# Kernel optimization log

Measured on AMD Instinct MI355X. Metric: run time of the kernel, lower is better.

## Reference

```python
import jax, jax.numpy as jnp
import numpy as np

B, T = 16, 40
NH, DEPTH, NCLASS, IMG_H, W_IMG = 128, 2, 6625, 32, 512
HIDDEN = 64  # nh < 256 -> hidden = 64
LINEAR_IN = NH * 8  # nh * int((32-3-1)/4+1)
BN_EPS = 1e-5


def _conv2d(x, w, b, stride, pad, groups=1):
    y = jax.lax.conv_general_dilated(
        x, w, (stride, stride), [(pad, pad), (pad, pad)],
        dimension_numbers=('NCHW', 'OIHW', 'NCHW'), feature_group_count=groups)
    return y + b[None, :, None, None]


def _conv_bn_act(x, w, b, g, bb, m, v, stride, pad, groups=1):
    y = _conv2d(x, w, b, stride, pad, groups)
    y = (y - m[None, :, None, None]) * jax.lax.rsqrt(v[None, :, None, None] + BN_EPS) \
        * g[None, :, None, None] + bb[None, :, None, None]
    return jax.nn.gelu(y, approximate=False)  # torch nn.GELU default = exact erf


def _gru(xs, wih, whh, bih, bhh):
    # torch GRU gate order: r, z, n. xs: [B, T, D] -> ys: [B, T, H]
    H = whh.shape[1]
    xp = jnp.einsum('btd,gd->btg', xs, wih) + bih  # [B,T,3H]

    def step(h, xt):
        hp = h @ whh.T + bhh
        r = jax.nn.sigmoid(xt[:, :H] + hp[:, :H])
        z = jax.nn.sigmoid(xt[:, H:2 * H] + hp[:, H:2 * H])
        n = jnp.tanh(xt[:, 2 * H:] + r * hp[:, 2 * H:])
        hn = (1.0 - z) * n + z * h
        return hn, hn

    h0 = jnp.zeros((xs.shape[0], H), xs.dtype)
    _, ys = jax.lax.scan(step, h0, jnp.swapaxes(xp, 0, 1))
    return jnp.swapaxes(ys, 0, 1)


def _forward(x, targets,
             conv0_w, conv0_b, bn0_g, bn0_b, bn0_m, bn0_v,
             blk_dw_w, blk_dw_b, blk_bn1_g, blk_bn1_b, blk_bn1_m, blk_bn1_v,
             blk_pw_w, blk_pw_b, blk_bn2_g, blk_bn2_b, blk_bn2_m, blk_bn2_v,
             enc_wih, enc_whh, enc_bih, enc_bhh,
             dec_wih, dec_whh, dec_bih, dec_bhh,
             emb, q_w, q_b, k_w, k_b, e_w, e_b, fc_w, fc_b):
    h = _conv_bn_act(x, conv0_w, conv0_b, bn0_g, bn0_b, bn0_m, bn0_v, 4, 0)  # [B,NH,8,128]
    # NOTE: original code applies each MicroBlock to the SAME x (feat = block(x)); faithful here.
    feat = h
    for i in range(DEPTH):
        t = h + _conv_bn_act(h, blk_dw_w[i], blk_dw_b[i], blk_bn1_g[i], blk_bn1_b[i],
                             blk_bn1_m[i], blk_bn1_v[i], 1, 1, groups=NH)
        feat = _conv_bn_act(t, blk_pw_w[i], blk_pw_b[i], blk_bn2_g[i], blk_bn2_b[i],
                            blk_bn2_m[i], blk_bn2_v[i], 1, 0)
    Bq, C, Hf, Wf = feat.shape
    feat_v = feat.reshape(Bq, C * Hf, Wf)  # Flatten(1,2)
    # adaptive_avg_pool1d target = W/4 == Wf -> identity
    feat_v = jnp.transpose(feat_v, (0, 2, 1))  # [B, Wf, C*Hf]
    enc = _gru(feat_v, enc_wih, enc_whh, enc_bih, enc_bhh)  # [B,Wf,H]
    out_enc = enc[:, -1:, :]  # [B,1,H]
    tgt = emb[targets]  # [B,T,H]
    in_dec = jnp.concatenate([out_enc, tgt], axis=1)  # [B,T+1,H]
    y = _gru(in_dec, dec_wih, dec_whh, dec_bih, dec_bhh)  # [B,T+1,H]
    q = y @ q_w.T + q_b  # [B,Td,NH]
    k = _conv2d(feat, k_w, k_b, 1, 1)  # [B,NH,h,w]
    t2 = jnp.tanh(k[:, None] + q[:, :, :, None, None])  # [B,Td,NH,h,w]
    e = jnp.einsum('btchw,c->bthw', t2, e_w[0]) + e_b[0]  # conv1x1_2: Linear(NH,1)
    a = jax.nn.softmax(e.reshape(Bq, e.shape[1], -1), axis=-1).reshape(e.shape)
    attn_feat = jnp.einsum('bchw,bthw->btc', feat, a)  # [B,Td,NH]
    # dropout: eval mode -> identity
    return attn_feat @ fc_w.T + fc_b  # [B,Td,NCLASS]


def setup_inputs() -> dict:
    key = jax.random.key(0)
    ks = iter(jax.random.split(key, 64))

    def rn(shape, s=0.05):
        return jax.random.normal(next(ks), shape, jnp.float32) * s

    inp = {
        'x': jax.random.normal(next(ks), (B, 3, IMG_H, W_IMG), jnp.float32),
        'targets': jax.random.randint(next(ks), (B, T), 0, NCLASS),
        'conv0_w': rn((NH, 3, 4, 4)), 'conv0_b': rn((NH,)),
        'bn0_g': jnp.ones((NH,)), 'bn0_b': jnp.zeros((NH,)),
        'bn0_m': jnp.zeros((NH,)), 'bn0_v': jnp.ones((NH,)),
        'blk_dw_w': rn((DEPTH, NH, 1, 3, 3)), 'blk_dw_b': rn((DEPTH, NH)),
        'blk_bn1_g': jnp.ones((DEPTH, NH)), 'blk_bn1_b': jnp.zeros((DEPTH, NH)),
        'blk_bn1_m': jnp.zeros((DEPTH, NH)), 'blk_bn1_v': jnp.ones((DEPTH, NH)),
        'blk_pw_w': rn((DEPTH, NH, NH, 1, 1)), 'blk_pw_b': rn((DEPTH, NH)),
        'blk_bn2_g': jnp.ones((DEPTH, NH)), 'blk_bn2_b': jnp.zeros((DEPTH, NH)),
        'blk_bn2_m': jnp.zeros((DEPTH, NH)), 'blk_bn2_v': jnp.ones((DEPTH, NH)),
        'enc_wih': rn((3 * HIDDEN, LINEAR_IN)), 'enc_whh': rn((3 * HIDDEN, HIDDEN)),
        'enc_bih': jnp.zeros((3 * HIDDEN,)), 'enc_bhh': jnp.zeros((3 * HIDDEN,)),
        'dec_wih': rn((3 * HIDDEN, HIDDEN)), 'dec_whh': rn((3 * HIDDEN, HIDDEN)),
        'dec_bih': jnp.zeros((3 * HIDDEN,)), 'dec_bhh': jnp.zeros((3 * HIDDEN,)),
        'emb': rn((NCLASS, HIDDEN)).at[1].set(0.0),  # padding_idx=1
        'q_w': rn((NH, HIDDEN)), 'q_b': jnp.zeros((NH,)),
        'k_w': rn((NH, NH, 3, 3)), 'k_b': jnp.zeros((NH,)),
        'e_w': rn((1, NH)), 'e_b': jnp.zeros((1,)),
        'fc_w': rn((NCLASS, NH)), 'fc_b': jnp.zeros((NCLASS,)),
    }
    return inp


def reference(x, targets,
              conv0_w, conv0_b, bn0_g, bn0_b, bn0_m, bn0_v,
              blk_dw_w, blk_dw_b, blk_bn1_g, blk_bn1_b, blk_bn1_m, blk_bn1_v,
              blk_pw_w, blk_pw_b, blk_bn2_g, blk_bn2_b, blk_bn2_m, blk_bn2_v,
              enc_wih, enc_whh, enc_bih, enc_bhh,
              dec_wih, dec_whh, dec_bih, dec_bhh,
              emb, q_w, q_b, k_w, k_b, e_w, e_b, fc_w, fc_b):
    return _forward(x, targets,
                    conv0_w, conv0_b, bn0_g, bn0_b, bn0_m, bn0_v,
                    blk_dw_w, blk_dw_b, blk_bn1_g, blk_bn1_b, blk_bn1_m, blk_bn1_v,
                    blk_pw_w, blk_pw_b, blk_bn2_g, blk_bn2_b, blk_bn2_m, blk_bn2_v,
                    enc_wih, enc_whh, enc_bih, enc_bhh,
                    dec_wih, dec_whh, dec_bih, dec_bhh,
                    emb, q_w, q_b, k_w, k_b, e_w, e_b, fc_w, fc_b)
```

## Files before the change

### kernel.cpp

```cpp
#include <hip/hip_runtime.h>
#include <hip/hip_bf16.h>

#define DEV __device__ __forceinline__

#define B_    16
#define T_    40
#define TDEC  41
#define NH    128
#define HF    8
#define WF    128
#define HID   64
#define G3    192
#define NCLS  6625
#define SPAT  1024
#define NFRAG 415

typedef _Float16 half8 __attribute__((ext_vector_type(8)));
typedef _Float16 half2_ __attribute__((ext_vector_type(2)));
typedef float    f32x4 __attribute__((ext_vector_type(4)));
typedef float    f32x2 __attribute__((ext_vector_type(2)));

#if __has_builtin(__builtin_amdgcn_fdot2)
#define FDOT2(w,h,acc) __builtin_amdgcn_fdot2((w),(h),(acc),false)
#else
#define FDOT2(w,h,acc) ((acc) + (float)((w)[0])*(float)((h)[0]) + (float)((w)[1])*(float)((h)[1]))
#endif

DEV float sigmoidf_(float x){ return 1.0f/(1.0f + __expf(-x)); }
DEV float tanhf_(float x){ float e = __expf(2.0f*x); return 1.0f - 2.0f/(e + 1.0f); }
DEV float gelu_(float x){ return 0.5f*x*(1.0f + erff(x*0.70710678118654752f)); }
DEV float bnf_(float x, float g, float b, float m, float v){
  return (x - m)*rsqrtf(v + 1e-5f)*g + b;
}

__global__ __launch_bounds__(256) void k_conv0(const float* __restrict__ x,
    const float* __restrict__ w, const float* __restrict__ bias,
    const float* __restrict__ bng, const float* __restrict__ bnb,
    const float* __restrict__ bnm, const float* __restrict__ bnv,
    float* __restrict__ h)
{
  int tid = blockIdx.x*256 + threadIdx.x;
  int ow = tid & 127;
  int oh = (tid >> 7) & 7;
  int c4 = (tid >> 10) & 31;
  int b  = tid >> 15;
  float acc[4] = {0.f,0.f,0.f,0.f};
  int xbase = ((b*3)*32 + oh*4)*512 + ow*4;
  for (int ci = 0; ci < 3; ++ci){
    #pragma unroll
    for (int kh = 0; kh < 4; ++kh){
      float4 xv = *(const float4*)(x + xbase + ci*(32*512) + kh*512);
      #pragma unroll
      for (int cc = 0; cc < 4; ++cc){
        int co = c4*4 + cc;
        const float* wp = w + ((co*3 + ci)*4 + kh)*4;
        acc[cc] += xv.x*wp[0] + xv.y*wp[1] + xv.z*wp[2] + xv.w*wp[3];
      }
    }
  }
  #pragma unroll
  for (int cc = 0; cc < 4; ++cc){
    int co = c4*4 + cc;
    float v = acc[cc] + bias[co];
    v = bnf_(v, bng[co], bnb[co], bnm[co], bnv[co]);
    h[((b*NH + co)*HF + oh)*WF + ow] = gelu_(v);
  }
}

__global__ __launch_bounds__(256) void k_dw(const float* __restrict__ h,
    const float* __restrict__ dww, const float* __restrict__ dwb,
    const float* __restrict__ g1, const float* __restrict__ b1,
    const float* __restrict__ m1, const float* __restrict__ v1,
    float* __restrict__ t)
{
  int tid = blockIdx.x*256 + threadIdx.x;
  int ow = tid & 127;
  int oh = (tid >> 7) & 7;
  int c  = (tid >> 10) & 127;
  int b  = tid >> 17;
  const float* wp = dww + NH*9 + c*9;
  const float* hp = h + ((b*NH + c)*HF)*WF;
  float acc = 0.f;
  #pragma unroll
  for (int kh = 0; kh < 3; ++kh){
    int ih = oh + kh - 1;
    if (ih < 0 || ih >= HF) continue;
    #pragma unroll
    for (int kw = 0; kw < 3; ++kw){
      int iw = ow + kw - 1;
      if (iw < 0 || iw >= WF) continue;
      acc += hp[ih*WF + iw]*wp[kh*3 + kw];
    }
  }
  float val = acc + dwb[NH + c];
  val = bnf_(val, g1[NH + c], b1[NH + c], m1[NH + c], v1[NH + c]);
  t[tid] = hp[oh*WF + ow] + gelu_(val);
}

__global__ __launch_bounds__(256) void k_fcprep(const float* __restrict__ fcw,
    _Float16* __restrict__ fcwH, _Float16* __restrict__ fcwL)
{
  int tid = blockIdx.x*256 + threadIdx.x;
  if (tid >= NFRAG*4*64*8) return;
  int j  = tid & 7;
  int l  = (tid >> 3) & 63;
  int kf = (tid >> 9) & 3;
  int nf = tid >> 11;
  int n = nf*16 + (l & 15);
  int k = kf*32 + ((l >> 4) << 3) + j;
  float v = (n < NCLS) ? fcw[n*NH + k] : 0.f;
  _Float16 hi = (_Float16)v;
  fcwH[tid] = hi;
  fcwL[tid] = (_Float16)(v - (float)hi);
}

__global__ __launch_bounds__(256) void k_misc(const float* __restrict__ pw,
    float* __restrict__ pwT, const float* __restrict__ kw,
    _Float16* __restrict__ kwA, const int* __restrict__ tgt,
    const float* __restrict__ emb, float* __restrict__ indec,
    const float* __restrict__ encwhh, unsigned* __restrict__ enc16,
    const float* __restrict__ decwhh, unsigned* __restrict__ dec16)
{
  int bid = blockIdx.x;
  if (bid < 64){
    int tid = bid*256 + threadIdx.x;
    int ci = tid & 127; int co = tid >> 7;
    pwT[ci*128 + co] = pw[16384 + co*128 + ci];
  } else if (bid < 640){
    int tid = (bid - 64)*256 + threadIdx.x;
    int j = tid & 7;
    int l = (tid >> 3) & 63;
    int f = (tid >> 9) & 7;
    int s = tid >> 12;
    int co = f*16 + (l & 15);
    int k  = s*32 + ((l >> 4) << 3) + j;
    int r  = k >> 7;
    int ci = k & 127;
    kwA[tid] = (_Float16)kw[(co*128 + ci)*9 + r];
  } else if (bid < 800){
    int tid = (bid - 640)*256 + threadIdx.x;
    if (tid >= B_*T_*HID) return;
    int j = tid & 63; int rest = tid >> 6;
    int t = rest % T_; int b = rest / T_;
    int cls = tgt[b*T_ + t];
    indec[(b*TDEC + 1 + t)*HID + j] = emb[cls*HID + j];
  } else {
    int seg = bid - 800;
    const float* src = (seg < 24) ? encwhh : decwhh;
    unsigned* dst    = (seg < 24) ? enc16   : dec16;
    int tid = (seg % 24)*256 + threadIdx.x;
    int r = tid >> 5; int k2 = tid & 31;
    half2_ hv;
    hv[0] = (_Float16)src[r*HID + 2*k2];
    hv[1] = (_Float16)src[r*HID + 2*k2 + 1];
    dst[tid] = __builtin_bit_cast(unsigned, hv);
  }
}

__global__ __launch_bounds__(512) void k_pw(const float* __restrict__ t,
    const float* __restrict__ pwT, const float* __restrict__ pwb,
    const float* __restrict__ g2, const float* __restrict__ b2,
    const float* __restrict__ m2, const float* __restrict__ v2,
    float* __restrict__ feat)
{
  int bid = blockIdx.x;
  int wh = bid & 1; int oh = (bid >> 1) & 7; int b = bid >> 4;
  int w0 = wh*64;
  int tid = threadIdx.x;
  __shared__ __align__(16) float tile[128*64];
  for (int i = 0; i < 16; ++i){
    int e = i*512 + tid; int ci = e >> 6; int wloc = e & 63;
    tile[ci*64 + wloc] = t[((b*NH + ci)*HF + oh)*WF + w0 + wloc];
  }
  __syncthreads();
  int co = tid & 127; int wq = tid >> 7;
  float acc[16];
  #pragma unroll
  for (int i = 0; i < 16; ++i) acc[i] = 0.f;
  for (int ci = 0; ci < 128; ++ci){
    float wt = pwT[ci*128 + co];
    const float4* tp = (const float4*)(tile + ci*64 + wq*16);
    #pragma unroll
    for (int j = 0; j < 4; ++j){
      float4 tv = tp[j];
      acc[j*4+0] += tv.x*wt; acc[j*4+1] += tv.y*wt;
      acc[j*4+2] += tv.z*wt; acc[j*4+3] += tv.w*wt;
    }
  }
  float bb = pwb[128 + co];
  float gg = g2[128 + co], bc = b2[128 + co], mm = m2[128 + co], vv = v2[128 + co];
  float* op = feat + ((b*NH + co)*HF + oh)*WF + w0 + wq*16;
  #pragma unroll
  for (int i = 0; i < 16; ++i){
    float v = bnf_(acc[i] + bb, gg, bc, mm, vv);
    op[i] = gelu_(v);
  }
}

__global__ __launch_bounds__(256) void k_encxp(const float* __restrict__ feat,
    const float* __restrict__ wih, const float* __restrict__ bih,
    float* __restrict__ xp)
{
  int m0 = blockIdx.x*32;
  int n0 = blockIdx.y*48;
  int b  = m0 >> 7;
  int w0 = m0 & 127;
  int tid = threadIdx.x;
  __shared__ float As[64*33];
  __shared__ float Bs[64*49];
  int tx = tid & 15, ty = tid >> 4;
  float acc[2][3] = {{0.f,0.f,0.f},{0.f,0.f,0.f}};
  for (int kt = 0; kt < 16; ++kt){
    int k0 = kt*64;
    #pragma unroll
    for (int i = 0; i < 8; ++i){
      int e = i*256 + tid; int kd = e >> 5; int mi = e & 31;
      int kg = k0 + kd;
      As[kd*33 + mi] = feat[((b*NH + (kg >> 3))*HF + (kg & 7))*WF + w0 + mi];
    }
    #pragma unroll
    for (int i = 0; i < 12; ++i){
      int e = i*256 + tid; int gi = e >> 6; int kd = e & 63;
      Bs[kd*49 + gi] = wih[(n0 + gi)*1024 + k0 + kd];
    }
    __syncthreads();
    for (int kd = 0; kd < 64; ++kd){
      float a0 = As[kd*33 + ty*2], a1 = As[kd*33 + ty*2 + 1];
      float b0 = Bs[kd*49 + tx*3], b1 = Bs[kd*49 + tx*3 + 1], b2 = Bs[kd*49 + tx*3 + 2];
      acc[0][0] += a0*b0; acc[0][1] += a0*b1; acc[0][2] += a0*b2;
      acc[1][0] += a1*b0; acc[1][1] += a1*b1; acc[1][2] += a1*b2;
    }
    __syncthreads();
  }
  #pragma unroll
  for (int i = 0; i < 2; ++i){
    int m = m0 + ty*2 + i;
    #pragma unroll
    for (int j = 0; j < 3; ++j){
      int g = n0 + tx*3 + j;
      xp[m*G3 + g] = acc[i][j] + bih[g];
    }
  }
}

template<int STEPS, bool WRITE_ALL>
__global__ __attribute__((amdgpu_waves_per_eu(1, 1))) __launch_bounds__(64)
void k_scan2(const float* __restrict__ xp, const uint4* __restrict__ whh16,
             const float* __restrict__ bhh, float* __restrict__ outp)
{
  __shared__ __align__(16) _Float16 hsh16[HID];
  int g = threadIdx.x;
  int b = blockIdx.x;
  uint4 w0q[8], w1q[8], w2q[8];
  const uint4* q0 = whh16 + g*8;
  const uint4* q1 = whh16 + (HID + g)*8;
  const uint4* q2 = whh16 + (2*HID + g)*8;
  #pragma unroll
  for (int k = 0; k < 8; ++k){ w0q[k] = q0[k]; w1q[k] = q1[k]; w2q[k] = q2[k]; }
  float b0 = bhh[g], b1 = bhh[HID + g], b2 = bhh[2*HID + g];
  float hg = 0.f;
  hsh16[g] = (_Float16)0.f;
  const float* xpb = xp + b*STEPS*G3;
  float x0a = xpb[g], x1a = xpb[HID + g], x2a = xpb[2*HID + g];
  float x0b = 0.f, x1b = 0.f, x2b = 0.f;
  if (STEPS > 1){
    const float* p = xpb + G3 + g;
    x0b = p[0]; x1b = p[HID]; x2b = p[2*HID];
  }
  for (int t = 0; t < STEPS; ++t){
    float x0c = 0.f, x1c = 0.f, x2c = 0.f;
    if (t + 2 < STEPS){
      const float* p = xpb + (t + 2)*G3 + g;
      x0c = p[0]; x1c = p[HID]; x2c = p[2*HID];
    }
    const uint4* h4 = (const uint4*)hsh16;
    float a0 = b0, a1 = b1, a2 = b2;
    float d0 = 0.f, d1 = 0.f, d2 = 0.f;
    #pragma unroll
    for (int i = 0; i < 8; i += 2){
      uint4 hvA = h4[i], hvB = h4[i+1];
      #define DO4(hv, wq, aa, bb, cc)                                          \
      { half2_ h0 = __builtin_bit_cast(half2_, hv.x);                          \
        half2_ h1 = __builtin_bit_cast(half2_, hv.y);                          \
        half2_ h2 = __builtin_bit_cast(half2_, hv.z);                          \
        half2_ h3 = __builtin_bit_cast(half2_, hv.w);                          \
        aa = FDOT2(__builtin_bit_cast(half2_, w0q[wq].x), h0, aa);             \
        bb = FDOT2(__builtin_bit_cast(half2_, w1q[wq].x), h0, bb);             \
        cc = FDOT2(__builtin_bit_cast(half2_, w2q[wq].x), h0, cc);             \
        aa = FDOT2(__builtin_bit_cast(half2_, w0q[wq].y), h1, aa);             \
        bb = FDOT2(__builtin_bit_cast(half2_, w1q[wq].y), h1, bb);             \
        cc = FDOT2(__builtin_bit_cast(half2_, w2q[wq].y), h1, cc);             \
        aa = FDOT2(__builtin_bit_cast(half2_, w0q[wq].z), h2, aa);             \
        bb = FDOT2(__builtin_bit_cast(half2_, w1q[wq].z), h2, bb);             \
        cc = FDOT2(__builtin_bit_cast(half2_, w2q[wq].z), h2, cc);             \
        aa = FDOT2(__builtin_bit_cast(half2_, w0q[wq].w), h3, aa);             \
        bb = FDOT2(__builtin_bit_cast(half2_, w1q[wq].w), h3, bb);             \
        cc = FDOT2(__builtin_bit_cast(half2_, w2q[wq].w), h3, cc); }
      DO4(hvA, i,   a0, a1, a2)
      DO4(hvB, i+1, d0, d1, d2)
      #undef DO4
    }
    float hp0 = a0 + d0;
    float hp1 = a1 + d1;
    float hp2 = a2 + d2;
    float e0 = __expf(-(x0a + hp0));
    float r  = __builtin_amdgcn_rcpf(1.0f + e0);
    float e1 = __expf(-(x1a + hp1));
    float z  = __builtin_amdgcn_rcpf(1.0f + e1);
    float ag = x2a + r*hp2;
    float ex = __expf(2.0f*ag);
    float n  = 1.0f - 2.0f*__builtin_amdgcn_rcpf(ex + 1.0f);
    hg = z*(hg - n) + n;
    if (WRITE_ALL) outp[(b*TDEC + t)*HID + g] = hg;
    hsh16[g] = (_Float16)hg;
    x0a = x0b; x1a = x1b; x2a = x2b;
    x0b = x0c; x1b = x1c; x2b = x2c;
  }
  if (!WRITE_ALL) outp[(b*TDEC)*HID + g] = hg;
}

__global__ __launch_bounds__(64) void k_kconv3(const float* __restrict__ feat,
    const uint4* __restrict__ kwA4, const float* __restrict__ kb,
    float* __restrict__ ko)
{
  int bid = blockIdx.x;
  int b  = ((bid & 7) << 1) | ((bid >> 3) & 1);
  int mq = (bid >> 4) & 3;
  int cs = (bid >> 6) & 3;
  int wq = (bid >> 8) & 1;
  int oh = (bid >> 9) & 7;
  int l  = threadIdx.x;
  int w0 = wq*64 + mq*16;
  int iwb = w0 + (l & 15);
  int cib = (l >> 4) << 3;

  f32x4 acc0{0.f,0.f,0.f,0.f}, acc1{0.f,0.f,0.f,0.f};
  uint4 a0A, a0B, a1A, a1B;
  float b0v[8], b1v[8];

  #define ISS(s, aX, aY, bvv) {                                               \
    aX = kwA4[(s)*512 + cs*128 + l];                                          \
    aY = kwA4[(s)*512 + cs*128 + 64 + l];                                     \
    int r = (s) >> 2; int dh = r/3 - 1; int dw2 = r%3 - 1;                    \
    int ci0 = ((s) & 3) << 5;                                                 \
    int ih = oh + dh; int iw = iwb + dw2;                                     \
    bool ok = (ih >= 0) & (ih < HF) & (iw >= 0) & (iw < WF);                  \
    const float* fp = feat + ((b*NH + ci0 + cib)*HF + ih)*WF + iw;            \
    _Pragma("unroll")                                                         \
    for (int jj = 0; jj < 8; ++jj) bvv[jj] = ok ? fp[jj*(HF*WF)] : 0.f;       \
  }
  #define CMP(aX, aY, bvv) {                                                  \
    half8 bf;                                                                 \
    _Pragma("unroll")                                                         \
    for (int jj = 0; jj < 8; ++jj) bf[jj] = (_Float16)bvv[jj];                \
    half8 af0 = __builtin_bit_cast(half8, aX);                                \
    half8 af1 = __builtin_bit_cast(half8, aY);                                \
    acc0 = __builtin_amdgcn_mfma_f32_16x16x32_f16(af0, bf, acc0, 0, 0, 0);    \
    acc1 = __builtin_amdgcn_mfma_f32_16x16x32_f16(af1, bf, acc1, 0, 0, 0);    \
  }

  ISS(0, a0A, a0B, b0v);
  for (int s = 0; s < 36; s += 2){
    if (s + 1 < 36) ISS(s + 1, a1A, a1B, b1v);
    CMP(a0A, a0B, b0v);
    if (s + 2 < 36) ISS(s + 2, a0A, a0B, b0v);
    if (s + 1 < 36) CMP(a1A, a1B, b1v);
  }
  #undef ISS
  #undef CMP

  int m = w0 + (l & 15);
  #pragma unroll
  for (int q = 0; q < 4; ++q){
    int co0 = cs*32 + ((l >> 4) << 2) + q;
    int co1 = co0 + 16;
    ko[((b*NH + co0)*HF + oh)*WF + m] = acc0[q] + kb[co0];
    ko[((b*NH + co1)*HF + oh)*WF + m] = acc1[q] + kb[co1];
  }
}

__global__ void k_xpd(const float* __restrict__ indec, const float* __restrict__ wih,
                      const float* __restrict__ bih, float* __restrict__ xpd)
{
  int tid = blockIdx.x*256 + threadIdx.x;
  if (tid >= B_*TDEC*G3) return;
  int g = tid % G3; int bt = tid / G3;
  const float4* r4 = (const float4*)(indec + bt*HID);
  const float4* w4 = (const float4*)(wih + g*HID);
  float acc = bih[g];
  #pragma unroll
  for (int j = 0; j < 16; ++j){
    float4 rv = r4[j], wv = w4[j];
    acc += rv.x*wv.x + rv.y*wv.y + rv.z*wv.z + rv.w*wv.w;
  }
  xpd[tid] = acc;
}

__global__ void k_q(const float* __restrict__ y, const float* __restrict__ qw,
                    const float* __restrict__ qb0, float* __restrict__ q)
{
  int tid = blockIdx.x*256 + threadIdx.x;
  if (tid >= B_*TDEC*NH) return;
  int co = tid & 127; int bt = tid >> 7;
  const float4* r4 = (const float4*)(y + bt*HID);
  const float4* w4 = (const float4*)(qw + co*HID);
  float acc = qb0[co];
  #pragma unroll
  for (int j = 0; j < 16; ++j){
    float4 rv = r4[j], wv = w4[j];
    acc += rv.x*wv.x + rv.y*wv.y + rv.z*wv.z + rv.w*wv.w;
  }
  q[tid] = acc;
}

__global__ __launch_bounds__(512) void k_e3(const float* __restrict__ k,
    const float* __restrict__ q, const float* __restrict__ ew,
    const float* __restrict__ eb, float* __restrict__ e)
{
  int bid = blockIdx.x;
  int st = bid & 15; int b = bid >> 4;
  int s0 = st*64;
  int tid = threadIdx.x;
  __shared__ float ksh[NH*64];
  __shared__ float qsh[TDEC*NH];
  __shared__ float ewsh[NH];
  #pragma unroll
  for (int i = 0; i < 16; ++i){
    int e2 = i*512 + tid; int c = e2 >> 6; int j = e2 & 63;
    ksh[e2] = k[(b*NH + c)*SPAT + s0 + j];
  }
  #pragma unroll
  for (int i = 0; i < 11; ++i){
    int e2 = i*512 + tid;
    if (e2 < TDEC*NH) qsh[e2] = q[b*TDEC*NH + e2];
  }
  if (tid < NH) ewsh[tid] = ew[tid];
  __syncthreads();
  int sl = tid & 63; int tp = tid >> 6;
  float ebv = eb[0];
  float acc[6] = {ebv, ebv, ebv, ebv, ebv, ebv};
  #pragma unroll 2
  for (int c = 0; c < NH; ++c){
    float kv = ksh[c*64 + sl];
    float ewc = ewsh[c];
    #pragma unroll
    for (int i = 0; i < 6; ++i){
      int t = tp + i*8;
      if (t < TDEC){
        float v = kv + qsh[t*NH + c];
        float ex = __expf(2.0f*v);
        float rc = __builtin_amdgcn_rcpf(ex + 1.0f);
        acc[i] += ewc*(1.0f - 2.0f*rc);
      }
    }
  }
  #pragma unroll
  for (int i = 0; i < 6; ++i){
    int t = tp + i*8;
    if (t < TDEC) e[(b*TDEC + t)*SPAT + s0 + sl] = acc[i];
  }
}

__global__ __launch_bounds__(256) void k_attnf2(const float* __restrict__ feat,
    const float* __restrict__ e, float* __restrict__ attnf)
{
  int bid = blockIdx.x;
  int ch = bid & 1; int rest = bid >> 1;
  int tq = rest % 11; int b = rest / 11;
  int tid = threadIdx.x;
  __shared__ __align__(16) float ash[4*SPAT];
  __shared__ float psh[4*4*64];
  __shared__ float sinv[4];
  for (int i = 0; i < 16; ++i){
    int e2 = i*256 + tid; int tt = e2 >> 10; int s = e2 & 1023;
    int t = tq*4 + tt;
    ash[e2] = (t < TDEC) ? e[(b*TDEC + t)*SPAT + s] : 0.f;
  }
  __syncthreads();
  {
    int w = tid >> 6; int l = tid & 63;
    float* row = ash + w*SPAT;
    float vreg[16];
    float mx = -1e30f;
    #pragma unroll
    for (int j = 0; j < 16; ++j){ vreg[j] = row[l + j*64]; mx = fmaxf(mx, vreg[j]); }
    #pragma unroll
    for (int m = 1; m < 64; m <<= 1) mx = fmaxf(mx, __shfl_xor(mx, m));
    float sum = 0.f;
    #pragma unroll
    for (int j = 0; j < 16; ++j){
      float ev = __expf(vreg[j] - mx);
      row[l + j*64] = ev;
      sum += ev;
    }
    #pragma unroll
    for (int m = 1; m < 64; m <<= 1) sum += __shfl_xor(sum, m);
    if (l == 0) sinv[w] = 1.0f/sum;
  }
  __syncthreads();
  int cl = tid & 63; int sq = tid >> 6;
  const float* fp = feat + (b*NH + ch*64 + cl)*SPAT + sq*256;
  float acc[4] = {0.f,0.f,0.f,0.f};
  for (int i = 0; i < 64; ++i){
    float4 fv = *(const float4*)(fp + i*4);
    #pragma unroll
    for (int tt = 0; tt < 4; ++tt){
      const float* ar = ash + tt*SPAT + sq*256 + i*4;
      acc[tt] += fv.x*ar[0] + fv.y*ar[1] + fv.z*ar[2] + fv.w*ar[3];
    }
  }
  #pragma unroll
  for (int tt = 0; tt < 4; ++tt) psh[(sq*4 + tt)*64 + cl] = acc[tt];
  __syncthreads();
  {
    int tt = tid >> 6; int c2 = tid & 63;
    int t = tq*4 + tt;
    if (t < TDEC){
      float v = psh[(0*4 + tt)*64 + c2] + psh[(1*4 + tt)*64 + c2]
              + psh[(2*4 + tt)*64 + c2] + psh[(3*4 + tt)*64 + c2];
      attnf[(b*TDEC + t)*NH + ch*64 + c2] = v*sinv[tt];
    }
  }
}

__global__ __launch_bounds__(256) void k_fc2(const float* __restrict__ attnf,
    const uint4* __restrict__ fcwH, const uint4* __restrict__ fcwL,
    const float* __restrict__ fcb, float* __restrict__ out)
{
  int mf = blockIdx.x;
  int ny = blockIdx.y;
  int tid = threadIdx.x;
  int l = tid & 63, w = tid >> 6;
  half8 ah[4], al[4];
  const float* ap = attnf + (mf*16 + (l & 15))*NH + ((l >> 4) << 3);
  #pragma unroll
  for (int kf = 0; kf < 4; ++kf){
    float4 v0 = *(const float4*)(ap + kf*32);
    float4 v1 = *(const float4*)(ap + kf*32 + 4);
    float vv[8] = {v0.x, v0.y, v0.z, v0.w, v1.x, v1.y, v1.z, v1.w};
    half8 h, lo;
    #pragma unroll
    for (int j = 0; j < 8; ++j){
      h[j]  = (_Float16)vv[j];
      lo[j] = (_Float16)(vv[j] - (float)h[j]);
    }
    ah[kf] = h; al[kf] = lo;
  }
  #pragma unroll
  for (int i = 0; i < 4; ++i){
    int nf = ny*16 + w*4 + i;
    if (nf >= NFRAG) return;
    f32x4 acc{0.f,0.f,0.f,0.f};
    #pragma unroll
    for (int kf = 0; kf < 4; ++kf){
      uint4 bH = fcwH[(nf*4 + kf)*64 + l];
      uint4 bL = fcwL[(nf*4 + kf)*64 + l];
      half8 wh = __builtin_bit_cast(half8, bH);
      half8 wl = __builtin_bit_cast(half8, bL);
      acc = __builtin_amdgcn_mfma_f32_16x16x32_f16(ah[kf], wh, acc, 0, 0, 0);
      acc = __builtin_amdgcn_mfma_f32_16x16x32_f16(al[kf], wh, acc, 0, 0, 0);
      acc = __builtin_amdgcn_mfma_f32_16x16x32_f16(ah[kf], wl, acc, 0, 0, 0);
    }
    int n = nf*16 + (l & 15);
    if (n < NCLS){
      float bias = fcb[n];
      int mrow = mf*16 + ((l >> 4) << 2);
      #pragma unroll
      for (int q = 0; q < 4; ++q)
        out[(mrow + q)*NCLS + n] = acc[q] + bias;
    }
  }
}

extern "C" void kernel_launch(void* const* d_in, const int* in_sizes, int n_in,
                              void* d_out, int out_size, void* d_ws, size_t ws_size,
                              hipStream_t stream)
{
  (void)in_sizes; (void)n_in; (void)out_size; (void)ws_size;
  const float* x      = (const float*)d_in[0];
  const int*   tgt    = (const int*)  d_in[1];
  const float* conv0w = (const float*)d_in[2];
  const float* conv0b = (const float*)d_in[3];
  const float* bn0g   = (const float*)d_in[4];
  const float* bn0b   = (const float*)d_in[5];
  const float* bn0m   = (const float*)d_in[6];
  const float* bn0v   = (const float*)d_in[7];
  const float* dww    = (const float*)d_in[8];
  const float* dwb    = (const float*)d_in[9];
  const float* bn1g   = (const float*)d_in[10];
  const float* bn1b   = (const float*)d_in[11];
  const float* bn1m   = (const float*)d_in[12];
  const float* bn1v   = (const float*)d_in[13];
  const float* pww    = (const float*)d_in[14];
  const float* pwb    = (const float*)d_in[15];
  const float* bn2g   = (const float*)d_in[16];
  const float* bn2b   = (const float*)d_in[17];
  const float* bn2m   = (const float*)d_in[18];
  const float* bn2v   = (const float*)d_in[19];
  const float* encwih = (const float*)d_in[20];
  const float* encwhh = (const float*)d_in[21];
  const float* encbih = (const float*)d_in[22];
  const float* encbhh = (const float*)d_in[23];
  const float* decwih = (const float*)d_in[24];
  const float* decwhh = (const float*)d_in[25];
  const float* decbih = (const float*)d_in[26];
  const float* decbhh = (const float*)d_in[27];
  const float* emb    = (const float*)d_in[28];
  const float* qw     = (const float*)d_in[29];
  const float* qb0    = (const float*)d_in[30];
  const float* kw     = (const float*)d_in[31];
  const float* kb     = (const float*)d_in[32];
  const float* ew     = (const float*)d_in[33];
  const float* eb     = (const float*)d_in[34];
  const float* fcw    = (const float*)d_in[35];
  const float* fcb    = (const float*)d_in[36];

  float* ws    = (float*)d_ws;
  float* hbuf  = ws + 0;
  float* tbuf  = ws + 2097152;
  float* feat  = ws + 4194304;
  float* xp    = ws + 6291456;
  float* indec = ws + 6684672;
  float* xpd   = ws + 6726656;
  float* ybuf  = ws + 6852608;
  float* qbuf  = ws + 6894592;
  float* attf  = ws + 6978560;
  float* pwT   = ws + 7062528;
  _Float16* kwA = (_Float16*)(ws + 7078912);
  unsigned* enc16 = (unsigned*)(ws + 7152640);
  unsigned* dec16 = (unsigned*)(ws + 7158784);
  _Float16* fcwH = (_Float16*)(ws + 7164928);
  _Float16* fcwL = (_Float16*)(ws + 7589888);
  float* kbuf  = hbuf;
  float* ebuf  = tbuf;
  float* out   = (float*)d_out;

  hipLaunchKernelGGL(k_conv0,   dim3(2048),        dim3(256), 0, stream,
                     x, conv0w, conv0b, bn0g, bn0b, bn0m, bn0v, hbuf);
  hipLaunchKernelGGL(k_dw,      dim3(8192),        dim3(256), 0, stream,
                     hbuf, dww, dwb, bn1g, bn1b, bn1m, bn1v, tbuf);
  hipLaunchKernelGGL(k_misc,    dim3(848),         dim3(256), 0, stream,
                     pww, pwT, kw, kwA, tgt, emb, indec,
                     encwhh, enc16, decwhh, dec16);
  hipLaunchKernelGGL(k_fcprep,  dim3(3320),        dim3(256), 0, stream,
                     fcw, fcwH, fcwL);
  hipLaunchKernelGGL(k_pw,      dim3(256),         dim3(512), 0, stream,
                     tbuf, pwT, pwb, bn2g, bn2b, bn2m, bn2v, feat);
  hipLaunchKernelGGL(k_encxp,   dim3(64, 4),       dim3(256), 0, stream,
                     feat, encwih, encbih, xp);
  hipLaunchKernelGGL((k_scan2<128,false>), dim3(16), dim3(64), 0, stream,
                     xp, (const uint4*)enc16, encbhh, indec);
  hipLaunchKernelGGL(k_kconv3,  dim3(4096),        dim3(64), 0, stream,
                     feat, (const uint4*)kwA, kb, kbuf);
  hipLaunchKernelGGL(k_xpd,     dim3(492),         dim3(256), 0, stream,
                     indec, decwih, decbih, xpd);
  hipLaunchKernelGGL((k_scan2<TDEC,true>), dim3(16), dim3(64), 0, stream,
                     xpd, (const uint4*)dec16, decbhh, ybuf);
  hipLaunchKernelGGL(k_q,       dim3(328),         dim3(256), 0, stream,
                     ybuf, qw, qb0, qbuf);
  hipLaunchKernelGGL(k_e3,      dim3(256),         dim3(512), 0, stream,
                     kbuf, qbuf, ew, eb, ebuf);
  hipLaunchKernelGGL(k_attnf2,  dim3(352),         dim3(256), 0, stream,
                     feat, ebuf, attf);
  hipLaunchKernelGGL(k_fc2,     dim3(41, 26),      dim3(256), 0, stream,
                     attf, (const uint4*)fcwH, (const uint4*)fcwL, fcb, out);
}
```

Baseline: 295.8 us.

## Compute encoder input projection with split-fp16 MFMA instead of scalar fp32 GEMM

Replaces the shared-memory fp32 tiled GEMM for the encoder GRU input projection with a one-wave-per-block MFMA kernel. The weights are pre-split into fp16 hi/lo parts in MFMA fragment layout inside the misc prep kernel. Activations are split on the fly, and three MFMAs per fragment recover near-fp32 accuracy. This targets ALU-bound scalar FMA cost. The trade-offs are only 128 single-wave blocks, more prep work, and reuse of the xpd/ybuf workspace regions for the split weights before those buffers are written.

```diff
diff --git a/kernel.cpp b/kernel.cpp
--- a/kernel.cpp
+++ b/kernel.cpp
@@ -119,7 +119,9 @@
     _Float16* __restrict__ kwA, const int* __restrict__ tgt,
     const float* __restrict__ emb, float* __restrict__ indec,
     const float* __restrict__ encwhh, unsigned* __restrict__ enc16,
-    const float* __restrict__ decwhh, unsigned* __restrict__ dec16)
+    const float* __restrict__ decwhh, unsigned* __restrict__ dec16,
+    const float* __restrict__ wih, _Float16* __restrict__ wihH,
+    _Float16* __restrict__ wihL)
 {
   int bid = blockIdx.x;
   if (bid < 64){
@@ -144,7 +146,7 @@
     int t = rest % T_; int b = rest / T_;
     int cls = tgt[b*T_ + t];
     indec[(b*TDEC + 1 + t)*HID + j] = emb[cls*HID + j];
-  } else {
+  } else if (bid < 848){
     int seg = bid - 800;
     const float* src = (seg < 24) ? encwhh : decwhh;
     unsigned* dst    = (seg < 24) ? enc16   : dec16;
@@ -154,6 +156,19 @@
     hv[0] = (_Float16)src[r*HID + 2*k2];
     hv[1] = (_Float16)src[r*HID + 2*k2 + 1];
     dst[tid] = __builtin_bit_cast(unsigned, hv);
+  } else {
+    int tid = (bid - 848)*256 + threadIdx.x;
+    if (tid >= 12*32*64*8) return;
+    int j  = tid & 7;
+    int l  = (tid >> 3) & 63;
+    int kf = (tid >> 9) & 31;
+    int nf = tid >> 14;
+    int n = nf*16 + (l & 15);
+    int k = kf*32 + ((l >> 4) << 3) + j;
+    float v = wih[n*1024 + k];
+    _Float16 hi = (_Float16)v;
+    wihH[tid] = hi;
+    wihL[tid] = (_Float16)(v - (float)hi);
   }
 }
 
@@ -197,49 +212,48 @@
   }
 }
 
-__global__ __launch_bounds__(256) void k_encxp(const float* __restrict__ feat,
-    const float* __restrict__ wih, const float* __restrict__ bih,
-    float* __restrict__ xp)
-{
-  int m0 = blockIdx.x*32;
-  int n0 = blockIdx.y*48;
-  int b  = m0 >> 7;
-  int w0 = m0 & 127;
-  int tid = threadIdx.x;
-  __shared__ float As[64*33];
-  __shared__ float Bs[64*49];
-  int tx = tid & 15, ty = tid >> 4;
-  float acc[2][3] = {{0.f,0.f,0.f},{0.f,0.f,0.f}};
-  for (int kt = 0; kt < 16; ++kt){
-    int k0 = kt*64;
-    #pragma unroll
-    for (int i = 0; i < 8; ++i){
-      int e = i*256 + tid; int kd = e >> 5; int mi = e & 31;
-      int kg = k0 + kd;
-      As[kd*33 + mi] = feat[((b*NH + (kg >> 3))*HF + (kg & 7))*WF + w0 + mi];
-    }
-    #pragma unroll
-    for (int i = 0; i < 12; ++i){
-      int e = i*256 + tid; int gi = e >> 6; int kd = e & 63;
-      Bs[kd*49 + gi] = wih[(n0 + gi)*1024 + k0 + kd];
-    }
-    __syncthreads();
-    for (int kd = 0; kd < 64; ++kd){
-      float a0 = As[kd*33 + ty*2], a1 = As[kd*33 + ty*2 + 1];
-      float b0 = Bs[kd*49 + tx*3], b1 = Bs[kd*49 + tx*3 + 1], b2 = Bs[kd*49 + tx*3 + 2];
-      acc[0][0] += a0*b0; acc[0][1] += a0*b1; acc[0][2] += a0*b2;
-      acc[1][0] += a1*b0; acc[1][1] += a1*b1; acc[1][2] += a1*b2;
-    }
-    __syncthreads();
-  }
-  #pragma unroll
-  for (int i = 0; i < 2; ++i){
-    int m = m0 + ty*2 + i;
-    #pragma unroll
-    for (int j = 0; j < 3; ++j){
-      int g = n0 + tx*3 + j;
-      xp[m*G3 + g] = acc[i][j] + bih[g];
-    }
+__global__ __launch_bounds__(64) void k_encxp2(const float* __restrict__ feat,
+    const uint4* __restrict__ wihH, const uint4* __restrict__ wihL,
+    const float* __restrict__ bih, float* __restrict__ xp)
+{
+  int mf = blockIdx.x;
+  int l  = threadIdx.x;
+  int b  = mf >> 3, wc = mf & 7;
+  int m_w = wc*16 + (l & 15);
+  f32x4 acc[12];
+  #pragma unroll
+  for (int nf = 0; nf < 12; ++nf) acc[nf] = (f32x4){0.f,0.f,0.f,0.f};
+  for (int kf = 0; kf < 32; ++kf){
+    int ci = kf*4 + (l >> 4);
+    const float* ap = feat + ((b*NH + ci)*HF)*WF + m_w;
+    float av[8];
+    #pragma unroll
+    for (int j = 0; j < 8; ++j) av[j] = ap[j*WF];
+    half8 ah, al;
+    #pragma unroll
+    for (int j = 0; j < 8; ++j){
+      ah[j] = (_Float16)av[j];
+      al[j] = (_Float16)(av[j] - (float)ah[j]);
+    }
+    #pragma unroll
+    for (int nf = 0; nf < 12; ++nf){
+      uint4 bH = wihH[(nf*32 + kf)*64 + l];
+      uint4 bL = wihL[(nf*32 + kf)*64 + l];
+      half8 wh = __builtin_bit_cast(half8, bH);
+      half8 wl = __builtin_bit_cast(half8, bL);
+      acc[nf] = __builtin_amdgcn_mfma_f32_16x16x32_f16(ah, wh, acc[nf], 0, 0, 0);
+      acc[nf] = __builtin_amdgcn_mfma_f32_16x16x32_f16(al, wh, acc[nf], 0, 0, 0);
+      acc[nf] = __builtin_amdgcn_mfma_f32_16x16x32_f16(ah, wl, acc[nf], 0, 0, 0);
+    }
+  }
+  int mbase = b*WF + wc*16 + ((l >> 4) << 2);
+  #pragma unroll
+  for (int nf = 0; nf < 12; ++nf){
+    int n = nf*16 + (l & 15);
+    float bias = bih[n];
+    #pragma unroll
+    for (int q = 0; q < 4; ++q)
+      xp[(mbase + q)*G3 + n] = acc[nf][q] + bias;
   }
 }
 
@@ -631,6 +645,8 @@
   unsigned* dec16 = (unsigned*)(ws + 7158784);
   _Float16* fcwH = (_Float16*)(ws + 7164928);
   _Float16* fcwL = (_Float16*)(ws + 7589888);
+  _Float16* wihH = (_Float16*)(ws + 6726656);
+  _Float16* wihL = (_Float16*)(ws + 6852608);
   float* kbuf  = hbuf;
   float* ebuf  = tbuf;
   float* out   = (float*)d_out;
@@ -639,15 +655,15 @@
                      x, conv0w, conv0b, bn0g, bn0b, bn0m, bn0v, hbuf);
   hipLaunchKernelGGL(k_dw,      dim3(8192),        dim3(256), 0, stream,
                      hbuf, dww, dwb, bn1g, bn1b, bn1m, bn1v, tbuf);
-  hipLaunchKernelGGL(k_misc,    dim3(848),         dim3(256), 0, stream,
+  hipLaunchKernelGGL(k_misc,    dim3(1616),        dim3(256), 0, stream,
                      pww, pwT, kw, kwA, tgt, emb, indec,
-                     encwhh, enc16, decwhh, dec16);
+                     encwhh, enc16, decwhh, dec16, encwih, wihH, wihL);
   hipLaunchKernelGGL(k_fcprep,  dim3(3320),        dim3(256), 0, stream,
                      fcw, fcwH, fcwL);
   hipLaunchKernelGGL(k_pw,      dim3(256),         dim3(512), 0, stream,
                      tbuf, pwT, pwb, bn2g, bn2b, bn2m, bn2v, feat);
-  hipLaunchKernelGGL(k_encxp,   dim3(64, 4),       dim3(256), 0, stream,
-                     feat, encwih, encbih, xp);
+  hipLaunchKernelGGL(k_encxp2,  dim3(128),         dim3(64), 0, stream,
+                     feat, (const uint4*)wihH, (const uint4*)wihL, encbih, xp);
   hipLaunchKernelGGL((k_scan2<128,false>), dim3(16), dim3(64), 0, stream,
                      xp, (const uint4*)enc16, encbhh, indec);
   hipLaunchKernelGGL(k_kconv3,  dim3(4096),        dim3(64), 0, stream,
```

New measurement: 370.2 us. 25.1% more time.
